# Kernel optimization log

Hardware: AMD Instinct MI355X
Metric: run time of the kernel (lower is better)

Reference implementation:

```python
import jax, jax.numpy as jnp
import numpy as np

C64 = jnp.complex64


def _ry(t):  # scalar angle -> [2,2] complex
    c = jnp.cos(t / 2).astype(C64)
    s = jnp.sin(t / 2).astype(C64)
    return jnp.stack([jnp.stack([c, -s]), jnp.stack([s, c])])


def _rz(t):  # scalar angle -> [2,2] complex (diagonal)
    p = jnp.exp(-0.5j * t.astype(C64))
    z = jnp.zeros((), C64)
    return jnp.stack([jnp.stack([p, z]), jnp.stack([z, jnp.conj(p)])])


def _rx_batch(t):  # t: [B] -> [B,2,2] complex (per-sample RX encoding gate)
    c = jnp.cos(t / 2).astype(C64)
    s = jnp.sin(t / 2).astype(C64)
    row0 = jnp.stack([c, -1j * s], axis=-1)
    row1 = jnp.stack([-1j * s, c], axis=-1)
    return jnp.stack([row0, row1], axis=-2)


def _apply_1q(state, gate, wire, n):
    # state: [B, 2^n]; wire 0 is the most significant bit (PennyLane convention)
    B = state.shape[0]
    pre, post = 2 ** wire, 2 ** (n - wire - 1)
    s = state.reshape(B, pre, 2, post)
    if gate.ndim == 2:
        s = jnp.einsum('ij,bpjq->bpiq', gate, s)
    else:  # per-sample gate [B,2,2]
        s = jnp.einsum('bij,bpjq->bpiq', gate, s)
    return s.reshape(B, -1)


def _apply_cnot(state, wire, n):
    # CNOT with control=wire, target=wire+1 (adjacent wires)
    B = state.shape[0]
    pre, post = 2 ** wire, 2 ** (n - wire - 2)
    s = state.reshape(B, pre, 2, 2, post)
    # control==1 block gets its target axis flipped
    s = jnp.concatenate([s[:, :, :1], s[:, :, 1:, ::-1]], axis=2)
    return s.reshape(B, -1)


def _circuit(x, params):
    # Batched statevector simulation of: RX(x_i) encoding, then n_layers of
    # (RY,RZ,RY) per wire + CNOT chain, then <Z_i> per wire.
    B, n = x.shape
    L = params.shape[0]
    state = jnp.zeros((B, 2 ** n), C64).at[:, 0].set(1.0)
    for i in range(n):
        state = _apply_1q(state, _rx_batch(x[:, i]), i, n)
    for l in range(L):
        for i in range(n):
            # RY(p0) first, then RZ(p1), then RY(p2): fuse into one 2x2 gate
            g = _ry(params[l, i, 2]) @ _rz(params[l, i, 1]) @ _ry(params[l, i, 0])
            state = _apply_1q(state, g, i, n)
        for i in range(n - 1):
            state = _apply_cnot(state, i, n)
    probs = jnp.abs(state) ** 2  # [B, 2^n] float32
    ez = []
    for i in range(n):
        p = probs.reshape(B, 2 ** i, 2, 2 ** (n - i - 1))
        ez.append(p[:, :, 0].sum((1, 2)) - p[:, :, 1].sum((1, 2)))
    return jnp.stack(ez, axis=1)  # [B, n]


def setup_inputs() -> dict:
    key = jax.random.key(0)
    k1, k2, k3, _ = jax.random.split(key, 4)
    B, n, L = 8192, 12, 3
    return {
        'x': jax.random.normal(k1, (B, n), jnp.float32),
        'params': jax.random.normal(k2, (L, n, 3), jnp.float32),
        'head_w': jax.random.normal(k3, (1, n), jnp.float32) / np.float32(np.sqrt(n)),
        'head_b': jnp.zeros((1,), jnp.float32),
    }


def reference(x, params, head_w, head_b):
    ez = _circuit(x, params)           # [B, n] per-wire Z expectations
    out = ez @ head_w.T + head_b       # Linear(n, 1)
    return out[:, 0]                   # squeeze(-1) -> [B]
```

## Files before the change

### kernel.cpp

```cpp
#include <hip/hip_runtime.h>
#include <math.h>

#define NQ 12
#define NTH 256
#define NL 3
#define GRID 1024

typedef _Float16 h8 __attribute__((ext_vector_type(8)));
typedef _Float16 h4 __attribute__((ext_vector_type(4)));
typedef float f4 __attribute__((ext_vector_type(4)));

#define MFMA __builtin_amdgcn_mfma_f32_16x16x32_f16


__device__ __forceinline__ int sfx(int v) {
    v ^= v >> 1; v ^= v >> 2; v ^= v >> 4; v ^= v >> 8;
    return v;
}
__device__ __forceinline__ int swzf(int off) {
    return off ^ (((((off >> 6) ^ (off >> 9)) & 7)) << 3);
}
__device__ __forceinline__ int swz1(int off) {
    return off ^ ((((off >> 5) ^ (off >> 9)) & 7) << 3);
}
__device__ __forceinline__ int swzw(int off) {
    return off ^ (((off >> 6) & 7) << 3);
}

__device__ __forceinline__ unsigned pk2(float lo, float hi) {
    auto t_ = __builtin_amdgcn_cvt_pkrtz(lo, hi);
    unsigned r_; __builtin_memcpy(&r_, &t_, 4); return r_;
}

__device__ __forceinline__ h8 xition(f4 re, f4 im) {
    unsigned a0 = pk2(re.x, re.y), a1 = pk2(re.z, re.w);
    unsigned b0 = pk2(im.x, im.y), b1 = pk2(im.z, im.w);
    asm("v_permlane32_swap_b32 %0, %1" : "+v"(a0), "+v"(b0));
    asm("v_permlane16_swap_b32 %0, %1" : "+v"(a0), "+v"(b0));
    asm("v_permlane32_swap_b32 %0, %1" : "+v"(a1), "+v"(b1));
    asm("v_permlane16_swap_b32 %0, %1" : "+v"(a1), "+v"(b1));
    union { unsigned u[4]; h8 v; } r_;
    r_.u[0] = a0; r_.u[1] = a1; r_.u[2] = b0; r_.u[3] = b1;
    return r_.v;
}

__global__ void __launch_bounds__(NTH, 4)
qsim_kernel(const float* __restrict__ x,
            const float* __restrict__ params,
            const float* __restrict__ head_w,
            const float* __restrict__ head_b,
            float* __restrict__ out, int Btot) {
    __shared__ __align__(16) _Float16 Sst[8192];
    __shared__ __align__(16) _Float16 Wl[6144];
    __shared__ float wlo[64], whi[64];
    __shared__ float csx[8 * 12], snx[8 * 12];
    __shared__ float Gs0[96];
    __shared__ __align__(16) float fct[48][2];
    __shared__ float wred[4];
    float* Gs = (float*)Sst;

    const int t = threadIdx.x, blk = blockIdx.x;

    if (t < 36) {
        float p0 = params[t * 3 + 0], p1 = params[t * 3 + 1], p2 = params[t * 3 + 2];
        float c0 = cosf(0.5f * p0), s0 = sinf(0.5f * p0);
        float ch = cosf(0.5f * p1), sh = sinf(0.5f * p1);
        float c2 = cosf(0.5f * p2), s2 = sinf(0.5f * p2);
        float pr_ = ch, pi = -sh, qr = ch, qi = sh;
        float A = c2 * c0, Bc = s2 * s0, Cc = c2 * s0, D = s2 * c0;
        float* g = &Gs[t * 8];
        g[0] = A * pr_ - Bc * qr;  g[1] = A * pi - Bc * qi;
        g[2] = -Cc * pr_ - D * qr; g[3] = -Cc * pi - D * qi;
        g[4] = D * pr_ + Cc * qr;  g[5] = D * pi + Cc * qi;
        g[6] = -Bc * pr_ + A * qr; g[7] = -Bc * pi + A * qi;
    }
    if (t < 64) {
        int v = t; float s = 0.f, s2 = 0.f;
#pragma unroll
        for (int be = 0; be < 6; ++be) {
            s  += ((v >> be) & 1) ? -head_w[11 - be] : head_w[11 - be];
            s2 += ((v >> be) & 1) ? -head_w[5 - be]  : head_w[5 - be];
        }
        wlo[v] = s; whi[v] = s2;
    }
    if (t >= 64 && t < 160) {
        int idx = t - 64;
        int pr = idx / 12, w = idx - pr * 12;
        int smp = blk + pr * GRID;
        if (smp < Btot) {
            float xv = 0.5f * x[smp * NQ + w];
            csx[pr * 12 + w] = cosf(xv);
            snx[pr * 12 + w] = sinf(xv);
        }
    }
    __syncthreads();

    if (t < 96) Gs0[t] = Gs[t];
#pragma unroll
    for (int i = 0; i < 24; ++i) {
        int e = i * 256 + t;
        int s = (e >> 10) + 3;
        int idx = e & 1023;
        int n = idx >> 5, k = idx & 31;
        int rp = n >> 4, tp = n & 15, rr = k >> 4, tt = k & 15;
        int l = s / 3, g = s - 3 * l;
        float ur = 1.f, ui = 0.f;
#pragma unroll
        for (int jj = 0; jj < 4; ++jj) {
            int wire = 11 - (4 * g + jj);
            const float* gp = &Gs[(l * 12 + wire) * 8];
            int rb = (tp >> jj) & 1, cb = (tt >> jj) & 1;
            float gr = gp[(rb * 2 + cb) * 2], gi = gp[(rb * 2 + cb) * 2 + 1];
            float nr = ur * gr - ui * gi;
            float ni = ur * gi + ui * gr;
            ur = nr; ui = ni;
        }
        float val = (rp == 0) ? ((rr == 0) ? ur : -ui)
                              : ((rr == 0) ? ui : ur);
        Wl[swzw(e)] = (_Float16)val;
    }
    __syncthreads();

    const int wv = t >> 6, u = t & 15, q = (t >> 4) & 3;
    const int wbs = swzw(u * 32 + q * 8);
    int g0b[4], g1b[4];
#pragma unroll
    for (int mb = 0; mb < 4; ++mb) {
        int m_ = wv * 64 + (u >> 2) * 16 + mb * 4 + (u & 3);
        g0b[mb] = swzf(m_ * 32 + q * 8);
        int l_ = t & 63;
        int m1 = ((l_ >> 2) & 3) * 64 + (l_ & 3) * 16 + wv * 4 + mb;
        g1b[mb] = swz1(m1 * 32 + q * 8);
    }
    const int sb = (t * 32) ^ (((t ^ (t >> 4)) & 7) << 3);

    const int s4 = (u ^ (u >> 1) ^ (u >> 2) ^ (u >> 3)) & 15;
    const int P4 = s4 & 1, q0 = q & 1, q1 = q >> 1;
    const int j7 = q1 ^ P4, j6 = q0 ^ q1 ^ P4;
    const int wv0 = wv & 1, wv1 = wv >> 1;
    int Eo[4], PwR[4];
#pragma unroll
    for (int r = 0; r < 4; ++r) {
        int r0 = r & 1, r1 = r >> 1;
        int j5 = r1 ^ j6, j4 = (r0 ^ r1) ^ j6;
        int j3 = wv1 ^ j4, j2 = wv0 ^ wv1 ^ j4;
        int m0 = s4 * 16 + j7 * 8 + j6 * 4 + j5 * 2 + j4;
        Eo[r]  = swzf(m0 * 32 + j3 * 8 + j2 * 4);
        PwR[r] = (wv0 ^ wv1 ^ j4);
    }
    const int Pw0 = wv0 ^ wv1 ^ j6;
    const int wloB = j6 * 48 + (wv1 ^ j6) * 8 + (wv0 ^ wv1 ^ j6) * 4 + Pw0 * 3;
    const float whiv = whi[s4 * 4 + j7 * 2 + j6];
    const f4 Z = {0.f, 0.f, 0.f, 0.f};

    const int iu = (t ^ (t >> 1)) & 0xFF;
    const int aI = iu >> 4;
    const int bI = 16 + (iu & 15);
    const int flip = (t & 1) << 3;

#define ST16(off_, va_, vb_) {                                               \
    union { unsigned u[4]; h8 v; } w_;                                       \
    w_.u[0] = pk2((va_).x, (va_).y); w_.u[1] = pk2((va_).z, (va_).w);        \
    w_.u[2] = pk2((vb_).x, (vb_).y); w_.u[3] = pk2((vb_).z, (vb_).w);        \
    *(h8*)&Sst[off_] = w_.v; }

#define PST1(CMP_, r_) {                                                     \
    bool pw_ = PwR[r_] != 0;                                                 \
    { float v0=eRA[0].CMP_, v1=eRA[1].CMP_, v2=eRA[2].CMP_, v3=eRA[3].CMP_;  \
      float a0_=pw_?v2:v0, a1_=pw_?v3:v1, a2_=pw_?v1:v3, a3_=pw_?v0:v2;      \
      union { unsigned u[2]; h4 v; } w_;                                     \
      w_.u[0]=pk2(a0_,a1_); w_.u[1]=pk2(a2_,a3_);                            \
      *(h4*)&Sst[Eo[r_]] = w_.v; }                                           \
    { float v0=eIA[0].CMP_, v1=eIA[1].CMP_, v2=eIA[2].CMP_, v3=eIA[3].CMP_;  \
      float a0_=pw_?v2:v0, a1_=pw_?v3:v1, a2_=pw_?v1:v3, a3_=pw_?v0:v2;      \
      union { unsigned u[2]; h4 v; } w_;                                     \
      w_.u[0]=pk2(a0_,a1_); w_.u[1]=pk2(a2_,a3_);                            \
      *(h4*)&Sst[Eo[r_] ^ 16] = w_.v; } }

#define RD1(CMP_, dr_) {                                                     \
    int b_ = wloB ^ (dr_);                                                   \
    float w0_ = whiv + wlo[b_],     w1_ = whiv + wlo[b_ ^ 1];                \
    float w2_ = whiv + wlo[b_ ^ 3], w3_ = whiv + wlo[b_ ^ 2];                \
    racc0 = fmaf(fmaf(eRA[0].CMP_, eRA[0].CMP_, eIA[0].CMP_*eIA[0].CMP_), w0_, racc0); \
    racc0 = fmaf(fmaf(eRA[1].CMP_, eRA[1].CMP_, eIA[1].CMP_*eIA[1].CMP_), w1_, racc0); \
    racc0 = fmaf(fmaf(eRA[2].CMP_, eRA[2].CMP_, eIA[2].CMP_*eIA[2].CMP_), w2_, racc0); \
    racc0 = fmaf(fmaf(eRA[3].CMP_, eRA[3].CMP_, eIA[3].CMP_*eIA[3].CMP_), w3_, racc0); }

#pragma unroll 1
    for (int pr = 0; ; ++pr) {
        const int smp = blk + pr * GRID;
        if (smp >= Btot) break;

        if (t < 48) {
            int k_ = t;
            int grp = k_ >> 4, h = k_ & 15;
            int wbase = (grp == 0) ? 3 : (grp == 1) ? 7 : 11;
            const float* cs_ = &csx[pr * 12];
            const float* sn_ = &snx[pr * 12];
            float ur = 1.f, ui = 0.f;
#pragma unroll
            for (int jj = 0; jj < 4; ++jj) {
                int w = wbase - jj;
                int bit = (h >> jj) & 1;
                const float* g = &Gs0[w * 8];
                float c = cs_[w], sn = sn_[w];
                float tr, ti;
                if (bit == 0) { tr = g[0] * c + g[3] * sn; ti = g[1] * c - g[2] * sn; }
                else          { tr = g[4] * c + g[7] * sn; ti = g[5] * c - g[6] * sn; }
                float nr = ur * tr - ui * ti, ni = ur * ti + ui * tr;
                ur = nr; ui = ni;
            }
            fct[k_][0] = ur; fct[k_][1] = ui;
        }
        __syncthreads();

        {
            float ar = fct[aI][0], ai = fct[aI][1];
            float br = fct[bI][0], bi = fct[bI][1];
            float abr = ar * br - ai * bi, abi = ar * bi + ai * br;
            float cr[16], ci[16];
#pragma unroll
            for (int k = 0; k < 16; ++k) {
                cr[k] = fct[32 + (k ^ flip)][0];
                ci[k] = fct[32 + (k ^ flip)][1];
            }
            float vr_[16], vi_[16];
#pragma unroll
            for (int tau = 0; tau < 16; ++tau) {
                const int cidx = tau ^ (tau >> 1);
                vr_[tau] = abr * cr[cidx] - abi * ci[cidx];
                vi_[tau] = abr * ci[cidx] + abi * cr[cidx];
            }
            union { unsigned u[4]; h8 v; } R0_, R1_, I0_, I1_;
#pragma unroll
            for (int k = 0; k < 4; ++k) {
                R0_.u[k] = pk2(vr_[2 * k],     vr_[2 * k + 1]);
                R1_.u[k] = pk2(vr_[8 + 2 * k], vr_[8 + 2 * k + 1]);
                I0_.u[k] = pk2(vi_[2 * k],     vi_[2 * k + 1]);
                I1_.u[k] = pk2(vi_[8 + 2 * k], vi_[8 + 2 * k + 1]);
            }
            const int off0 = t * 32;
            *(h8*)&Sst[swzf(off0)]      = R0_.v;
            *(h8*)&Sst[swzf(off0 + 8)]  = R1_.v;
            *(h8*)&Sst[swzf(off0 + 16)] = I0_.v;
            *(h8*)&Sst[swzf(off0 + 24)] = I1_.v;
        }

        float racc0 = 0.f;
#pragma unroll
        for (int l = 1; l < NL; ++l) {
            {
                const int sW = ((l - 1) * 3 + 0) * 1024;
                h8 bf0 = *(const h8*)&Wl[sW + wbs];
                h8 bf1 = *(const h8*)&Wl[sW + 512 + wbs];
                h8 aA[4];
#pragma unroll
                for (int mb = 0; mb < 4; ++mb)
                    aA[mb] = *(const h8*)&Sst[g0b[mb]];
                f4 cR[4], cI[4];
#pragma unroll
                for (int mb = 0; mb < 4; ++mb) {
                    cR[mb] = MFMA(aA[mb], bf0, Z, 0, 0, 0);
                    cI[mb] = MFMA(aA[mb], bf1, Z, 0, 0, 0);
                }
                ST16(sb,      cR[0], cR[1]) ST16(sb ^ 8,  cR[2], cR[3])
                ST16(sb ^ 16, cI[0], cI[1]) ST16(sb ^ 24, cI[2], cI[3])
                __syncthreads();
            }
            {
                const int sW1 = ((l - 1) * 3 + 1) * 1024, sW2 = ((l - 1) * 3 + 2) * 1024;
                h8 bg0 = *(const h8*)&Wl[sW1 + wbs];
                h8 bg1 = *(const h8*)&Wl[sW1 + 512 + wbs];
                h8 bh0 = *(const h8*)&Wl[sW2 + wbs];
                h8 bh1 = *(const h8*)&Wl[sW2 + 512 + wbs];
                h8 gA[4];
#pragma unroll
                for (int mb = 0; mb < 4; ++mb)
                    gA[mb] = *(const h8*)&Sst[g1b[mb]];
                if (l < NL - 1) __syncthreads();
                f4 eRA[4], eIA[4];
                {
                    f4 dR[4], dI[4]; h8 t2[4];
#pragma unroll
                    for (int mb = 0; mb < 4; ++mb) {
                        dR[mb] = MFMA(gA[mb], bg0, Z, 0, 0, 0);
                        dI[mb] = MFMA(gA[mb], bg1, Z, 0, 0, 0);
                    }
#pragma unroll
                    for (int mb = 0; mb < 4; ++mb) t2[mb] = xition(dR[mb], dI[mb]);
#pragma unroll
                    for (int mb = 0; mb < 4; ++mb) {
                        eRA[mb] = MFMA(t2[mb], bh0, Z, 0, 0, 0);
                        eIA[mb] = MFMA(t2[mb], bh1, Z, 0, 0, 0);
                    }
                }
                if (l < NL - 1) {
                    PST1(x, 0) PST1(y, 1) PST1(z, 2) PST1(w, 3)
                    __syncthreads();
                } else {
                    RD1(x, 0) RD1(y, 31) RD1(z, 63) RD1(w, 32)
                }
            }
        }
#pragma unroll
        for (int o = 32; o >= 1; o >>= 1)
            racc0 += __shfl_xor(racc0, o, 64);
        if ((t & 63) == 0) wred[wv] = racc0;
        __syncthreads();
        if (t == 0) {
            float r = head_b[0];
#pragma unroll
            for (int i2 = 0; i2 < 4; ++i2) r += wred[i2];
            out[smp] = r;
        }
    }
}

extern "C" void kernel_launch(void* const* d_in, const int* in_sizes, int n_in,
                              void* d_out, int out_size, void* d_ws, size_t ws_size,
                              hipStream_t stream) {
    const float* x = (const float*)d_in[0];
    const float* params = (const float*)d_in[1];
    const float* head_w = (const float*)d_in[2];
    const float* head_b = (const float*)d_in[3];
    float* out = (float*)d_out;
    int B = in_sizes[0] / NQ;

    hipLaunchKernelGGL(qsim_kernel, dim3(GRID), dim3(NTH), 0, stream,
                       x, params, head_w, head_b, out, B);
}
```

Before: 104.9 us.

## Process two samples per block with 512 threads sharing gate tables

Doubles the block to 512 threads so each block simulates two samples at once, with each half of the waves owning a separate statevector slice in shared memory. Grid shrinks to 768 blocks and the per-block setup (fused-gate weight table, head weights) is amortised over twice as many samples per iteration. The cost is doubled shared-memory state per block, which may limit how many blocks fit per CU, and block-wide barriers now also synchronise the two independent samples.

```diff
diff --git a/kernel.cpp b/kernel.cpp
--- a/kernel.cpp
+++ b/kernel.cpp
@@ -2,9 +2,9 @@
 #include <math.h>
 
 #define NQ 12
-#define NTH 256
+#define NTH 512
 #define NL 3
-#define GRID 1024
+#define GRID 768
 
 typedef _Float16 h8 __attribute__((ext_vector_type(8)));
 typedef _Float16 h4 __attribute__((ext_vector_type(4)));
@@ -44,22 +44,23 @@
     return r_.v;
 }
 
-__global__ void __launch_bounds__(NTH, 4)
+__global__ void __launch_bounds__(NTH, 6)
 qsim_kernel(const float* __restrict__ x,
             const float* __restrict__ params,
             const float* __restrict__ head_w,
             const float* __restrict__ head_b,
             float* __restrict__ out, int Btot) {
-    __shared__ __align__(16) _Float16 Sst[8192];
+    __shared__ __align__(16) _Float16 Sst[16384];
     __shared__ __align__(16) _Float16 Wl[6144];
     __shared__ float wlo[64], whi[64];
-    __shared__ float csx[8 * 12], snx[8 * 12];
+    __shared__ float csx[6 * 24], snx[6 * 24];
     __shared__ float Gs0[96];
-    __shared__ __align__(16) float fct[48][2];
-    __shared__ float wred[4];
+    __shared__ __align__(16) float fct[2][48][2];
+    __shared__ float wred[8];
     float* Gs = (float*)Sst;
 
     const int t = threadIdx.x, blk = blockIdx.x;
+    const int npairs = (Btot + 1) >> 1;
 
     if (t < 36) {
         float p0 = params[t * 3 + 0], p1 = params[t * 3 + 1], p2 = params[t * 3 + 2];
@@ -83,22 +84,26 @@
         }
         wlo[v] = s; whi[v] = s2;
     }
-    if (t >= 64 && t < 160) {
+    if (t >= 64 && t < 208) {
         int idx = t - 64;
-        int pr = idx / 12, w = idx - pr * 12;
-        int smp = blk + pr * GRID;
-        if (smp < Btot) {
-            float xv = 0.5f * x[smp * NQ + w];
-            csx[pr * 12 + w] = cosf(xv);
-            snx[pr * 12 + w] = sinf(xv);
+        int pr = idx / 24, w = idx - pr * 24;
+        int pairIdx = blk + pr * GRID;
+        if (pairIdx < npairs) {
+            int smp = pairIdx * 2 + (w >= 12 ? 1 : 0);
+            int wire = (w >= 12) ? (w - 12) : w;
+            if (smp < Btot) {
+                float xv = 0.5f * x[smp * NQ + wire];
+                csx[pr * 24 + w] = cosf(xv);
+                snx[pr * 24 + w] = sinf(xv);
+            }
         }
     }
     __syncthreads();
 
     if (t < 96) Gs0[t] = Gs[t];
 #pragma unroll
-    for (int i = 0; i < 24; ++i) {
-        int e = i * 256 + t;
+    for (int i = 0; i < 12; ++i) {
+        int e = i * 512 + t;
         int s = (e >> 10) + 3;
         int idx = e & 1023;
         int n = idx >> 5, k = idx & 31;
@@ -122,22 +127,25 @@
     __syncthreads();
 
     const int wv = t >> 6, u = t & 15, q = (t >> 4) & 3;
+    const int sid = wv >> 2, w4 = wv & 3;
+    const int SOFF = sid * 8192;
+    const int t4 = t & 255;
     const int wbs = swzw(u * 32 + q * 8);
     int g0b[4], g1b[4];
 #pragma unroll
     for (int mb = 0; mb < 4; ++mb) {
-        int m_ = wv * 64 + (u >> 2) * 16 + mb * 4 + (u & 3);
-        g0b[mb] = swzf(m_ * 32 + q * 8);
+        int m_ = w4 * 64 + (u >> 2) * 16 + mb * 4 + (u & 3);
+        g0b[mb] = swzf(m_ * 32 + q * 8) + SOFF;
         int l_ = t & 63;
-        int m1 = ((l_ >> 2) & 3) * 64 + (l_ & 3) * 16 + wv * 4 + mb;
-        g1b[mb] = swz1(m1 * 32 + q * 8);
-    }
-    const int sb = (t * 32) ^ (((t ^ (t >> 4)) & 7) << 3);
+        int m1 = ((l_ >> 2) & 3) * 64 + (l_ & 3) * 16 + w4 * 4 + mb;
+        g1b[mb] = swz1(m1 * 32 + q * 8) + SOFF;
+    }
+    const int sb = ((t4 * 32) ^ (((t4 ^ (t4 >> 4)) & 7) << 3)) + SOFF;
 
     const int s4 = (u ^ (u >> 1) ^ (u >> 2) ^ (u >> 3)) & 15;
     const int P4 = s4 & 1, q0 = q & 1, q1 = q >> 1;
     const int j7 = q1 ^ P4, j6 = q0 ^ q1 ^ P4;
-    const int wv0 = wv & 1, wv1 = wv >> 1;
+    const int wv0 = w4 & 1, wv1 = w4 >> 1;
     int Eo[4], PwR[4];
 #pragma unroll
     for (int r = 0; r < 4; ++r) {
@@ -145,7 +153,7 @@
         int j5 = r1 ^ j6, j4 = (r0 ^ r1) ^ j6;
         int j3 = wv1 ^ j4, j2 = wv0 ^ wv1 ^ j4;
         int m0 = s4 * 16 + j7 * 8 + j6 * 4 + j5 * 2 + j4;
-        Eo[r]  = swzf(m0 * 32 + j3 * 8 + j2 * 4);
+        Eo[r]  = swzf(m0 * 32 + j3 * 8 + j2 * 4) + SOFF;
         PwR[r] = (wv0 ^ wv1 ^ j4);
     }
     const int Pw0 = wv0 ^ wv1 ^ j6;
@@ -153,10 +161,10 @@
     const float whiv = whi[s4 * 4 + j7 * 2 + j6];
     const f4 Z = {0.f, 0.f, 0.f, 0.f};
 
-    const int iu = (t ^ (t >> 1)) & 0xFF;
+    const int iu = (t4 ^ (t4 >> 1)) & 0xFF;
     const int aI = iu >> 4;
     const int bI = 16 + (iu & 15);
-    const int flip = (t & 1) << 3;
+    const int flip = (t4 & 1) << 3;
 
 #define ST16(off_, va_, vb_) {                                               \
     union { unsigned u[4]; h8 v; } w_;                                       \
@@ -188,15 +196,15 @@
 
 #pragma unroll 1
     for (int pr = 0; ; ++pr) {
-        const int smp = blk + pr * GRID;
-        if (smp >= Btot) break;
-
-        if (t < 48) {
-            int k_ = t;
+        const int pairIdx = blk + pr * GRID;
+        if (pairIdx >= npairs) break;
+
+        if (t < 96) {
+            int s_ = t / 48, k_ = t - s_ * 48;
             int grp = k_ >> 4, h = k_ & 15;
             int wbase = (grp == 0) ? 3 : (grp == 1) ? 7 : 11;
-            const float* cs_ = &csx[pr * 12];
-            const float* sn_ = &snx[pr * 12];
+            const float* cs_ = &csx[pr * 24 + s_ * 12];
+            const float* sn_ = &snx[pr * 24 + s_ * 12];
             float ur = 1.f, ui = 0.f;
 #pragma unroll
             for (int jj = 0; jj < 4; ++jj) {
@@ -210,19 +218,19 @@
                 float nr = ur * tr - ui * ti, ni = ur * ti + ui * tr;
                 ur = nr; ui = ni;
             }
-            fct[k_][0] = ur; fct[k_][1] = ui;
+            fct[s_][k_][0] = ur; fct[s_][k_][1] = ui;
         }
         __syncthreads();
 
         {
-            float ar = fct[aI][0], ai = fct[aI][1];
-            float br = fct[bI][0], bi = fct[bI][1];
+            float ar = fct[sid][aI][0], ai = fct[sid][aI][1];
+            float br = fct[sid][bI][0], bi = fct[sid][bI][1];
             float abr = ar * br - ai * bi, abi = ar * bi + ai * br;
             float cr[16], ci[16];
 #pragma unroll
             for (int k = 0; k < 16; ++k) {
-                cr[k] = fct[32 + (k ^ flip)][0];
-                ci[k] = fct[32 + (k ^ flip)][1];
+                cr[k] = fct[sid][32 + (k ^ flip)][0];
+                ci[k] = fct[sid][32 + (k ^ flip)][1];
             }
             float vr_[16], vi_[16];
 #pragma unroll
@@ -239,11 +247,11 @@
                 I0_.u[k] = pk2(vi_[2 * k],     vi_[2 * k + 1]);
                 I1_.u[k] = pk2(vi_[8 + 2 * k], vi_[8 + 2 * k + 1]);
             }
-            const int off0 = t * 32;
-            *(h8*)&Sst[swzf(off0)]      = R0_.v;
-            *(h8*)&Sst[swzf(off0 + 8)]  = R1_.v;
-            *(h8*)&Sst[swzf(off0 + 16)] = I0_.v;
-            *(h8*)&Sst[swzf(off0 + 24)] = I1_.v;
+            const int off0 = t4 * 32;
+            *(h8*)&Sst[swzf(off0)      + SOFF] = R0_.v;
+            *(h8*)&Sst[swzf(off0 + 8)  + SOFF] = R1_.v;
+            *(h8*)&Sst[swzf(off0 + 16) + SOFF] = I0_.v;
+            *(h8*)&Sst[swzf(off0 + 24) + SOFF] = I1_.v;
         }
 
         float racc0 = 0.f;
@@ -307,11 +315,14 @@
             racc0 += __shfl_xor(racc0, o, 64);
         if ((t & 63) == 0) wred[wv] = racc0;
         __syncthreads();
-        if (t == 0) {
-            float r = head_b[0];
-#pragma unroll
-            for (int i2 = 0; i2 < 4; ++i2) r += wred[i2];
-            out[smp] = r;
+        if (t < 2) {
+            int smp = pairIdx * 2 + t;
+            if (smp < Btot) {
+                float r = head_b[0];
+#pragma unroll
+                for (int i2 = 0; i2 < 4; ++i2) r += wred[t * 4 + i2];
+                out[smp] = r;
+            }
         }
     }
 }
```

Result: slower. 130.5 us (+24.4%).

## Assign one sample per wavefront with private LDS state, removing block barriers

Applied to the files above, without the earlier changes.

Each wavefront now simulates its own sample in a private 8K-half LDS buffer instead of all four waves cooperating on one sample. This removes the __syncthreads between gate stages and the cross-wave reduction. The grid is halved and each block handles 16 samples in a fixed 4-iteration loop. LDS use per block grows about fourfold and occupancy is lowered to 2 blocks per CU, so latency hiding comes from independent waves rather than from more blocks. The loop is hard-wired to 4 iterations with GRID 512, which covers exactly B=8192, so larger batches would be left uncomputed.

```diff
diff --git a/kernel.cpp b/kernel.cpp
--- a/kernel.cpp
+++ b/kernel.cpp
@@ -4,7 +4,7 @@
 #define NQ 12
 #define NTH 256
 #define NL 3
-#define GRID 1024
+#define GRID 512
 
 typedef _Float16 h8 __attribute__((ext_vector_type(8)));
 typedef _Float16 h4 __attribute__((ext_vector_type(4)));
@@ -44,20 +44,19 @@
     return r_.v;
 }
 
-__global__ void __launch_bounds__(NTH, 4)
+__global__ void __launch_bounds__(NTH, 2)
 qsim_kernel(const float* __restrict__ x,
             const float* __restrict__ params,
             const float* __restrict__ head_w,
             const float* __restrict__ head_b,
             float* __restrict__ out, int Btot) {
-    __shared__ __align__(16) _Float16 Sst[8192];
+    __shared__ __align__(16) _Float16 Sst[4][8192];
     __shared__ __align__(16) _Float16 Wl[6144];
     __shared__ float wlo[64], whi[64];
-    __shared__ float csx[8 * 12], snx[8 * 12];
+    __shared__ float csx[16 * 12], snx[16 * 12];
     __shared__ float Gs0[96];
-    __shared__ __align__(16) float fct[48][2];
-    __shared__ float wred[4];
-    float* Gs = (float*)Sst;
+    __shared__ __align__(16) float fct[4][48][2];
+    float* Gs = (float*)&Sst[0][0];
 
     const int t = threadIdx.x, blk = blockIdx.x;
 
@@ -83,14 +82,14 @@
         }
         wlo[v] = s; whi[v] = s2;
     }
-    if (t >= 64 && t < 160) {
+    if (t >= 64) {
         int idx = t - 64;
-        int pr = idx / 12, w = idx - pr * 12;
-        int smp = blk + pr * GRID;
+        int slot = idx / 12, w = idx - slot * 12;
+        int smp = (slot >> 2) * (GRID * 4) + blk * 4 + (slot & 3);
         if (smp < Btot) {
             float xv = 0.5f * x[smp * NQ + w];
-            csx[pr * 12 + w] = cosf(xv);
-            snx[pr * 12 + w] = sinf(xv);
+            csx[slot * 12 + w] = cosf(xv);
+            snx[slot * 12 + w] = sinf(xv);
         }
     }
     __syncthreads();
@@ -121,82 +120,59 @@
     }
     __syncthreads();
 
-    const int wv = t >> 6, u = t & 15, q = (t >> 4) & 3;
+    const int wv = t >> 6, lane = t & 63, u = t & 15, q = (t >> 4) & 3;
+    _Float16* Ss = &Sst[wv][0];
     const int wbs = swzw(u * 32 + q * 8);
-    int g0b[4], g1b[4];
-#pragma unroll
-    for (int mb = 0; mb < 4; ++mb) {
-        int m_ = wv * 64 + (u >> 2) * 16 + mb * 4 + (u & 3);
-        g0b[mb] = swzf(m_ * 32 + q * 8);
-        int l_ = t & 63;
-        int m1 = ((l_ >> 2) & 3) * 64 + (l_ & 3) * 16 + wv * 4 + mb;
-        g1b[mb] = swz1(m1 * 32 + q * 8);
-    }
-    const int sb = (t * 32) ^ (((t ^ (t >> 4)) & 7) << 3);
-
     const int s4 = (u ^ (u >> 1) ^ (u >> 2) ^ (u >> 3)) & 15;
     const int P4 = s4 & 1, q0 = q & 1, q1 = q >> 1;
     const int j7 = q1 ^ P4, j6 = q0 ^ q1 ^ P4;
-    const int wv0 = wv & 1, wv1 = wv >> 1;
-    int Eo[4], PwR[4];
-#pragma unroll
-    for (int r = 0; r < 4; ++r) {
-        int r0 = r & 1, r1 = r >> 1;
-        int j5 = r1 ^ j6, j4 = (r0 ^ r1) ^ j6;
-        int j3 = wv1 ^ j4, j2 = wv0 ^ wv1 ^ j4;
-        int m0 = s4 * 16 + j7 * 8 + j6 * 4 + j5 * 2 + j4;
-        Eo[r]  = swzf(m0 * 32 + j3 * 8 + j2 * 4);
-        PwR[r] = (wv0 ^ wv1 ^ j4);
-    }
-    const int Pw0 = wv0 ^ wv1 ^ j6;
-    const int wloB = j6 * 48 + (wv1 ^ j6) * 8 + (wv0 ^ wv1 ^ j6) * 4 + Pw0 * 3;
     const float whiv = whi[s4 * 4 + j7 * 2 + j6];
     const f4 Z = {0.f, 0.f, 0.f, 0.f};
-
-    const int iu = (t ^ (t >> 1)) & 0xFF;
-    const int aI = iu >> 4;
-    const int bI = 16 + (iu & 15);
-    const int flip = (t & 1) << 3;
 
 #define ST16(off_, va_, vb_) {                                               \
     union { unsigned u[4]; h8 v; } w_;                                       \
     w_.u[0] = pk2((va_).x, (va_).y); w_.u[1] = pk2((va_).z, (va_).w);        \
     w_.u[2] = pk2((vb_).x, (vb_).y); w_.u[3] = pk2((vb_).z, (vb_).w);        \
-    *(h8*)&Sst[off_] = w_.v; }
-
-#define PST1(CMP_, r_) {                                                     \
-    bool pw_ = PwR[r_] != 0;                                                 \
+    *(h8*)&Ss[off_] = w_.v; }
+
+#define PSTX(CMP_, r0_, r1_) {                                               \
+    int j5_ = (r1_) ^ j6, j4_ = ((r0_) ^ (r1_)) ^ j6;                        \
+    int j3_ = wv1 ^ j4_, j2_ = wv0 ^ wv1 ^ j4_;                              \
+    int m0_ = s4 * 16 + j7 * 8 + j6 * 4 + j5_ * 2 + j4_;                     \
+    int Eo_ = swzf(m0_ * 32 + j3_ * 8 + j2_ * 4);                            \
+    bool pw_ = ((wv0 ^ wv1 ^ j4_) != 0);                                     \
     { float v0=eRA[0].CMP_, v1=eRA[1].CMP_, v2=eRA[2].CMP_, v3=eRA[3].CMP_;  \
       float a0_=pw_?v2:v0, a1_=pw_?v3:v1, a2_=pw_?v1:v3, a3_=pw_?v0:v2;      \
       union { unsigned u[2]; h4 v; } w_;                                     \
       w_.u[0]=pk2(a0_,a1_); w_.u[1]=pk2(a2_,a3_);                            \
-      *(h4*)&Sst[Eo[r_]] = w_.v; }                                           \
+      *(h4*)&Ss[Eo_] = w_.v; }                                               \
     { float v0=eIA[0].CMP_, v1=eIA[1].CMP_, v2=eIA[2].CMP_, v3=eIA[3].CMP_;  \
       float a0_=pw_?v2:v0, a1_=pw_?v3:v1, a2_=pw_?v1:v3, a3_=pw_?v0:v2;      \
       union { unsigned u[2]; h4 v; } w_;                                     \
       w_.u[0]=pk2(a0_,a1_); w_.u[1]=pk2(a2_,a3_);                            \
-      *(h4*)&Sst[Eo[r_] ^ 16] = w_.v; } }
-
-#define RD1(CMP_, dr_) {                                                     \
-    int b_ = wloB ^ (dr_);                                                   \
+      *(h4*)&Ss[Eo_ ^ 16] = w_.v; } }
+
+#define RDX(CMP_, dr_) {                                                     \
+    int b_ = wloB_ ^ (dr_);                                                  \
     float w0_ = whiv + wlo[b_],     w1_ = whiv + wlo[b_ ^ 1];                \
     float w2_ = whiv + wlo[b_ ^ 3], w3_ = whiv + wlo[b_ ^ 2];                \
-    racc0 = fmaf(fmaf(eRA[0].CMP_, eRA[0].CMP_, eIA[0].CMP_*eIA[0].CMP_), w0_, racc0); \
-    racc0 = fmaf(fmaf(eRA[1].CMP_, eRA[1].CMP_, eIA[1].CMP_*eIA[1].CMP_), w1_, racc0); \
-    racc0 = fmaf(fmaf(eRA[2].CMP_, eRA[2].CMP_, eIA[2].CMP_*eIA[2].CMP_), w2_, racc0); \
-    racc0 = fmaf(fmaf(eRA[3].CMP_, eRA[3].CMP_, eIA[3].CMP_*eIA[3].CMP_), w3_, racc0); }
+    racc = fmaf(fmaf(eRA[0].CMP_, eRA[0].CMP_, eIA[0].CMP_*eIA[0].CMP_), w0_, racc); \
+    racc = fmaf(fmaf(eRA[1].CMP_, eRA[1].CMP_, eIA[1].CMP_*eIA[1].CMP_), w1_, racc); \
+    racc = fmaf(fmaf(eRA[2].CMP_, eRA[2].CMP_, eIA[2].CMP_*eIA[2].CMP_), w2_, racc); \
+    racc = fmaf(fmaf(eRA[3].CMP_, eRA[3].CMP_, eIA[3].CMP_*eIA[3].CMP_), w3_, racc); }
 
 #pragma unroll 1
-    for (int pr = 0; ; ++pr) {
-        const int smp = blk + pr * GRID;
-        if (smp >= Btot) break;
-
-        if (t < 48) {
-            int k_ = t;
+    for (int pr = 0; pr < 4; ++pr) {
+        const int smp = (pr * GRID + blk) * 4 + wv;
+        if (smp >= Btot) continue;
+
+        if (lane < 48) {
+            int k_ = lane;
             int grp = k_ >> 4, h = k_ & 15;
             int wbase = (grp == 0) ? 3 : (grp == 1) ? 7 : 11;
-            const float* cs_ = &csx[pr * 12];
-            const float* sn_ = &snx[pr * 12];
+            const int slot = pr * 4 + wv;
+            const float* cs_ = &csx[slot * 12];
+            const float* sn_ = &snx[slot * 12];
             float ur = 1.f, ui = 0.f;
 #pragma unroll
             for (int jj = 0; jj < 4; ++jj) {
@@ -210,19 +186,23 @@
                 float nr = ur * tr - ui * ti, ni = ur * ti + ui * tr;
                 ur = nr; ui = ni;
             }
-            fct[k_][0] = ur; fct[k_][1] = ui;
-        }
-        __syncthreads();
-
-        {
-            float ar = fct[aI][0], ai = fct[aI][1];
-            float br = fct[bI][0], bi = fct[bI][1];
+            fct[wv][k_][0] = ur; fct[wv][k_][1] = ui;
+        }
+
+#pragma unroll
+        for (int mx = 0; mx < 4; ++mx) {
+            const int m = mx * 64 + lane;
+            const int iu_ = (m ^ (m >> 1)) & 0xFF;
+            const int aI_ = iu_ >> 4, bI_ = 16 + (iu_ & 15);
+            const int flip_ = (m & 1) << 3;
+            float ar = fct[wv][aI_][0], ai = fct[wv][aI_][1];
+            float br = fct[wv][bI_][0], bi = fct[wv][bI_][1];
             float abr = ar * br - ai * bi, abi = ar * bi + ai * br;
             float cr[16], ci[16];
 #pragma unroll
-            for (int k = 0; k < 16; ++k) {
-                cr[k] = fct[32 + (k ^ flip)][0];
-                ci[k] = fct[32 + (k ^ flip)][1];
+            for (int k2 = 0; k2 < 16; k2 += 2) {
+                f4 v = *(const f4*)&fct[wv][32 + (k2 ^ flip_)][0];
+                cr[k2] = v.x; ci[k2] = v.y; cr[k2 + 1] = v.z; ci[k2 + 1] = v.w;
             }
             float vr_[16], vi_[16];
 #pragma unroll
@@ -239,33 +219,39 @@
                 I0_.u[k] = pk2(vi_[2 * k],     vi_[2 * k + 1]);
                 I1_.u[k] = pk2(vi_[8 + 2 * k], vi_[8 + 2 * k + 1]);
             }
-            const int off0 = t * 32;
-            *(h8*)&Sst[swzf(off0)]      = R0_.v;
-            *(h8*)&Sst[swzf(off0 + 8)]  = R1_.v;
-            *(h8*)&Sst[swzf(off0 + 16)] = I0_.v;
-            *(h8*)&Sst[swzf(off0 + 24)] = I1_.v;
-        }
-
-        float racc0 = 0.f;
+            const int off0 = m * 32;
+            *(h8*)&Ss[swzf(off0)]      = R0_.v;
+            *(h8*)&Ss[swzf(off0 + 8)]  = R1_.v;
+            *(h8*)&Ss[swzf(off0 + 16)] = I0_.v;
+            *(h8*)&Ss[swzf(off0 + 24)] = I1_.v;
+        }
+
+        float racc = 0.f;
 #pragma unroll
         for (int l = 1; l < NL; ++l) {
             {
                 const int sW = ((l - 1) * 3 + 0) * 1024;
                 h8 bf0 = *(const h8*)&Wl[sW + wbs];
                 h8 bf1 = *(const h8*)&Wl[sW + 512 + wbs];
-                h8 aA[4];
-#pragma unroll
-                for (int mb = 0; mb < 4; ++mb)
-                    aA[mb] = *(const h8*)&Sst[g0b[mb]];
-                f4 cR[4], cI[4];
-#pragma unroll
-                for (int mb = 0; mb < 4; ++mb) {
-                    cR[mb] = MFMA(aA[mb], bf0, Z, 0, 0, 0);
-                    cI[mb] = MFMA(aA[mb], bf1, Z, 0, 0, 0);
+#pragma unroll
+                for (int wvx = 0; wvx < 4; ++wvx) {
+                    h8 aA[4];
+#pragma unroll
+                    for (int mb = 0; mb < 4; ++mb) {
+                        int m_ = wvx * 64 + (u >> 2) * 16 + mb * 4 + (u & 3);
+                        aA[mb] = *(const h8*)&Ss[swzf(m_ * 32 + q * 8)];
+                    }
+                    f4 cR[4], cI[4];
+#pragma unroll
+                    for (int mb = 0; mb < 4; ++mb) {
+                        cR[mb] = MFMA(aA[mb], bf0, Z, 0, 0, 0);
+                        cI[mb] = MFMA(aA[mb], bf1, Z, 0, 0, 0);
+                    }
+                    const int tx = wvx * 64 + lane;
+                    const int sb_ = (tx * 32) ^ (((tx ^ (tx >> 4)) & 7) << 3);
+                    ST16(sb_,      cR[0], cR[1]) ST16(sb_ ^ 8,  cR[2], cR[3])
+                    ST16(sb_ ^ 16, cI[0], cI[1]) ST16(sb_ ^ 24, cI[2], cI[3])
                 }
-                ST16(sb,      cR[0], cR[1]) ST16(sb ^ 8,  cR[2], cR[3])
-                ST16(sb ^ 16, cI[0], cI[1]) ST16(sb ^ 24, cI[2], cI[3])
-                __syncthreads();
             }
             {
                 const int sW1 = ((l - 1) * 3 + 1) * 1024, sW2 = ((l - 1) * 3 + 2) * 1024;
@@ -273,46 +259,46 @@
                 h8 bg1 = *(const h8*)&Wl[sW1 + 512 + wbs];
                 h8 bh0 = *(const h8*)&Wl[sW2 + wbs];
                 h8 bh1 = *(const h8*)&Wl[sW2 + 512 + wbs];
-                h8 gA[4];
-#pragma unroll
-                for (int mb = 0; mb < 4; ++mb)
-                    gA[mb] = *(const h8*)&Sst[g1b[mb]];
-                if (l < NL - 1) __syncthreads();
-                f4 eRA[4], eIA[4];
-                {
+                h8 gA[16];
+#pragma unroll
+                for (int wvx = 0; wvx < 4; ++wvx)
+#pragma unroll
+                    for (int mb = 0; mb < 4; ++mb) {
+                        int m1 = ((lane >> 2) & 3) * 64 + (lane & 3) * 16 + wvx * 4 + mb;
+                        gA[wvx * 4 + mb] = *(const h8*)&Ss[swz1(m1 * 32 + q * 8)];
+                    }
+#pragma unroll
+                for (int wvx = 0; wvx < 4; ++wvx) {
                     f4 dR[4], dI[4]; h8 t2[4];
 #pragma unroll
                     for (int mb = 0; mb < 4; ++mb) {
-                        dR[mb] = MFMA(gA[mb], bg0, Z, 0, 0, 0);
-                        dI[mb] = MFMA(gA[mb], bg1, Z, 0, 0, 0);
+                        dR[mb] = MFMA(gA[wvx * 4 + mb], bg0, Z, 0, 0, 0);
+                        dI[mb] = MFMA(gA[wvx * 4 + mb], bg1, Z, 0, 0, 0);
                     }
 #pragma unroll
                     for (int mb = 0; mb < 4; ++mb) t2[mb] = xition(dR[mb], dI[mb]);
+                    f4 eRA[4], eIA[4];
 #pragma unroll
                     for (int mb = 0; mb < 4; ++mb) {
                         eRA[mb] = MFMA(t2[mb], bh0, Z, 0, 0, 0);
                         eIA[mb] = MFMA(t2[mb], bh1, Z, 0, 0, 0);
                     }
+                    const int wv0 = wvx & 1, wv1 = wvx >> 1;
+                    if (l < NL - 1) {
+                        PSTX(x, 0, 0) PSTX(y, 1, 0) PSTX(z, 0, 1) PSTX(w, 1, 1)
+                    } else {
+                        const int Pw0_ = wv0 ^ wv1 ^ j6;
+                        const int wloB_ = j6 * 48 + (wv1 ^ j6) * 8 +
+                                          (wv0 ^ wv1 ^ j6) * 4 + Pw0_ * 3;
+                        RDX(x, 0) RDX(y, 31) RDX(z, 63) RDX(w, 32)
+                    }
                 }
-                if (l < NL - 1) {
-                    PST1(x, 0) PST1(y, 1) PST1(z, 2) PST1(w, 3)
-                    __syncthreads();
-                } else {
-                    RD1(x, 0) RD1(y, 31) RD1(z, 63) RD1(w, 32)
-                }
             }
         }
 #pragma unroll
         for (int o = 32; o >= 1; o >>= 1)
-            racc0 += __shfl_xor(racc0, o, 64);
-        if ((t & 63) == 0) wred[wv] = racc0;
-        __syncthreads();
-        if (t == 0) {
-            float r = head_b[0];
-#pragma unroll
-            for (int i2 = 0; i2 < 4; ++i2) r += wred[i2];
-            out[smp] = r;
-        }
+            racc += __shfl_xor(racc, o, 64);
+        if (lane == 0) out[smp] = head_b[0] + racc;
     }
 }
 
```

After: 117.7 us. 12.2% more time.
